# Performance work log

Hardware: AMD Instinct MI355X
Metric: run time of the kernel (lower is better)

Reference implementation:

```python
import jax, jax.numpy as jnp
import numpy as np

C = 256
RED = 8
CR = C // RED  # 32
B, H, W = 4, 64, 64
EPS = 1e-5


def setup_inputs() -> dict:
    key = jax.random.key(0)
    ks = jax.random.split(key, 12)
    s = 0.05
    return {
        "x": jax.random.normal(ks[0], (B, C, H, W), dtype=jnp.float32),
        "Wq": jax.random.normal(ks[1], (CR, C), dtype=jnp.float32) * s,
        "bq": jax.random.normal(ks[2], (CR,), dtype=jnp.float32) * s,
        "Wk": jax.random.normal(ks[3], (CR, C), dtype=jnp.float32) * s,
        "bk": jax.random.normal(ks[4], (CR,), dtype=jnp.float32) * s,
        "Wv": jax.random.normal(ks[5], (C, C), dtype=jnp.float32) * s,
        "bv": jax.random.normal(ks[6], (C,), dtype=jnp.float32) * s,
        "Wo": jax.random.normal(ks[7], (C, C), dtype=jnp.float32) * s,
        "bo": jax.random.normal(ks[8], (C,), dtype=jnp.float32) * s,
        "gamma": jnp.ones((C,), dtype=jnp.float32),
        "beta": jnp.zeros((C,), dtype=jnp.float32),
        "running_mean": jax.random.normal(ks[9], (C,), dtype=jnp.float32) * s,
        "running_var": jax.random.uniform(ks[10], (C,), dtype=jnp.float32, minval=0.5, maxval=1.5),
    }


def reference(x, Wq, bq, Wk, bk, Wv, bv, Wo, bo, gamma, beta, running_mean, running_var):
    b, c, h, w = x.shape
    n = h * w
    scale = c ** (-0.5)  # use_scale=True: in_channels**-0.5
    xf = x.reshape(b, c, n)  # [B, C, N]
    # 1x1 convs == per-pixel channel matmuls
    q = jnp.einsum('oc,bcn->bon', Wq, xf) + bq[None, :, None]   # [B, CR, N]
    k = jnp.einsum('oc,bcn->bon', Wk, xf) + bk[None, :, None]   # [B, CR, N]
    v = jnp.einsum('oc,bcn->bon', Wv, xf) + bv[None, :, None]   # [B, C, N]
    # attention[b, q_pos, k_pos], softmax over key positions (dim=2)
    attn = jnp.einsum('bcq,bck->bqk', q, k) * scale             # [B, N, N]
    attn = jax.nn.softmax(attn, axis=2)
    # out[b, c, q_pos] = sum_k v[b, c, k] * attn[b, q_pos, k]
    out = jnp.einsum('bck,bqk->bcq', v, attn)                   # [B, C, N]
    out = jnp.einsum('oc,bcn->bon', Wo, out) + bo[None, :, None]
    # BatchNorm2d (inference: running stats)
    inv = gamma / jnp.sqrt(running_var + EPS)
    out = out * inv[None, :, None] + (beta - running_mean * inv)[None, :, None]
    out = out.reshape(b, c, h, w)
    return jax.nn.relu(out + x)
```

## Files before the change

### kernel.cpp

```cpp
#include <hip/hip_runtime.h>
#include <hip/hip_bf16.h>

typedef unsigned short u16;
typedef unsigned int u32;

#define B_ 4
#define C_ 256
#define N_ 4096

constexpr float C1 = 0.09016844005556021f;

typedef float f32x16 __attribute__((ext_vector_type(16)));
typedef short bf16x8 __attribute__((ext_vector_type(8)));
typedef u32 u32x4 __attribute__((ext_vector_type(4)));
typedef int i32x2 __attribute__((ext_vector_type(2)));

__device__ __forceinline__ u16 bf16r(float f) {
    union { float f; u32 u; } a; a.f = f;
    u32 u = a.u;
    u += 0x7fffu + ((u >> 16) & 1u);
    return (u16)(u >> 16);
}

__device__ __forceinline__ float bf2f(u16 h) {
    union { u32 u; float f; } a; a.u = ((u32)h) << 16; return a.f;
}

__device__ __forceinline__ u32 pk2(float a, float b) {
    __hip_bfloat162 h = __float22bfloat162_rn(make_float2(a, b));
    union { __hip_bfloat162 h; u32 u; } c; c.h = h;
    return c.u;
}

__device__ __forceinline__ u32 cvtpk(float lo, float hi) {
    u32 r;
    asm("v_cvt_pk_bf16_f32 %0, %1, %2" : "=v"(r) : "v"(lo), "v"(hi));
    return r;
}

__device__ __forceinline__ void swap32(u32 &a, u32 &b) {
#if __has_builtin(__builtin_amdgcn_permlane32_swap)
    i32x2 r = __builtin_amdgcn_permlane32_swap((int)a, (int)b, false, false);
    a = (u32)r.x; b = (u32)r.y;
#else
    u32 as = __shfl_xor(a, 32), bs = __shfl_xor(b, 32);
    int hi = (threadIdx.x & 32) ? 1 : 0;
    u32 na = hi ? bs : a;
    u32 nb = hi ? b : as;
    a = na; b = nb;
#endif
}

__device__ __forceinline__ bf16x8 ld8(const u16* p) {
    return *reinterpret_cast<const bf16x8*>(p);
}

__device__ __forceinline__ void gld_lds16(const u16* g, u16* lbase, int lane) {
#if __has_builtin(__builtin_amdgcn_global_load_lds)
    __builtin_amdgcn_global_load_lds(
        (const __attribute__((address_space(1))) void*)g,
        (__attribute__((address_space(3))) void*)lbase, 16, 0, 0);
#else
    *reinterpret_cast<bf16x8*>(lbase + lane * 8) = ld8(g);
#endif
}

__device__ __forceinline__ int crow(int r, int hi) { return (r & 3) + 8 * (r >> 2) + 4 * hi; }

__global__ __launch_bounds__(256) void prep(
    const float* __restrict__ Wq, const float* __restrict__ Wk,
    const float* __restrict__ Wv, const float* __restrict__ Wo,
    const float* __restrict__ bo, const float* __restrict__ gamma,
    const float* __restrict__ beta, const float* __restrict__ rm, const float* __restrict__ rv,
    u16* __restrict__ wqk, u16* __restrict__ wv_b, u16* __restrict__ wo_b,
    float* __restrict__ scale, float* __restrict__ shift)
{
    int i = blockIdx.x * 256 + threadIdx.x;
    if (i < 16384) {
        float w = (i < 8192) ? Wq[i] * C1 : Wk[i - 8192];
        wqk[i] = bf16r(w);
    } else if (i < 81920) {
        wv_b[i - 16384] = bf16r(Wv[i - 16384]);
    } else if (i < 147456) {
        wo_b[i - 81920] = bf16r(Wo[i - 81920]);
    } else if (i < 147712) {
        int o = i - 147456;
        float inv = gamma[o] * rsqrtf(rv[o] + 1e-5f);
        scale[o] = inv;
        shift[o] = beta[o] + (bo[o] - rm[o]) * inv;
    }
}

__global__ __launch_bounds__(512) void projf(
    const float* __restrict__ x, const u16* __restrict__ wqk, const u16* __restrict__ wv,
    const float* __restrict__ bq, const float* __restrict__ bk, const float* __restrict__ bv,
    u16* __restrict__ qkt, u16* __restrict__ vout)
{
    __shared__ u16 xt[64 * 256];
    int tid = threadIdx.x;
    int lane = tid & 63, wid = tid >> 6;
    int r31 = lane & 31, hi = lane >> 5;
    int b = blockIdx.y, n0 = blockIdx.x * 64;
    const float* xb = x + (size_t)b * C_ * N_ + n0;
#pragma unroll
    for (int i = 0; i < 16; ++i) {
        int c2 = i * 8 + wid;
        int n = lane;
        float a0 = xb[(size_t)(2 * c2) * N_ + n];
        float a1 = xb[(size_t)(2 * c2 + 1) * N_ + n];
        int slot = (c2 >> 2) ^ (n & 31);
        *reinterpret_cast<u32*>(&xt[n * 256 + slot * 8 + (c2 & 3) * 2]) = pk2(a0, a1);
    }
    __syncthreads();
    for (int i = 0; i < 3; ++i) {
        int t = wid + i * 8;
        if (t < 20) {
            bool isqk = (t < 4);
            int nb = isqk ? (t >> 1) * 32 : ((t - 4) & 1) * 32;
            int gb = isqk ? (t & 1) * 32 : ((t - 4) >> 1) * 32;
            const u16* grow = (isqk ? wqk : wv) + (size_t)(gb + r31) * C_ + hi * 8;
            f32x16 acc;
#pragma unroll
            for (int r = 0; r < 16; ++r) acc[r] = 0.f;
#pragma unroll
            for (int ks = 0; ks < 16; ++ks) {
                int slot = (2 * ks + hi) ^ r31;
                bf16x8 lf = ld8(&xt[(nb + r31) * 256 + slot * 8]);
                bf16x8 gf = ld8(grow + ks * 16);
                if (isqk) acc = __builtin_amdgcn_mfma_f32_32x32x16_bf16(lf, gf, acc, 0, 0, 0);
                else      acc = __builtin_amdgcn_mfma_f32_32x32x16_bf16(gf, lf, acc, 0, 0, 0);
            }
            if (isqk) {
                int o = gb + r31;
                float bias = (o < 32) ? bq[o] * C1 : bk[o - 32];
                u16* qrow = qkt + ((size_t)b * N_ + n0 + nb) * 64 + o;
#pragma unroll
                for (int r = 0; r < 16; ++r)
                    qrow[(size_t)crow(r, hi) * 64] = bf16r(acc[r] + bias);
            } else {
                u16* vb = vout + (size_t)b * C_ * N_ + n0 + nb + r31;
#pragma unroll
                for (int r = 0; r < 16; ++r) {
                    int c = gb + crow(r, hi);
                    vb[(size_t)c * N_] = bf16r(acc[r] + bv[c]);
                }
            }
        }
    }
}

__global__ __launch_bounds__(512, 4) void attn(
    const u16* __restrict__ qkt, const u16* __restrict__ v,
    u16* __restrict__ opart, float* __restrict__ lpart, int kts)
{
    __shared__ u16 vt[2][128 * 128];
    __shared__ u16 ktt[2][16 * 128];
    int tid = threadIdx.x;
    int lane = tid & 63, wid = tid >> 6;
    int r31 = lane & 31, hi = lane >> 5;

    int nwg = 32 * 4 * gridDim.z;
    int wgl = blockIdx.x + 32 * (blockIdx.y + 4 * blockIdx.z);
    int cpx = nwg >> 3;
    int swzid = (wgl & 7) * cpx + (wgl >> 3);
    int bx = swzid & 31;
    int by = (swzid >> 5) & 3;
    int bz = swzid >> 7;

    int b = by, zs = bz;
    int q0 = bx * 128 + (wid >> 1) * 32;
    int cb = (wid & 1) * 128;
    const u16* qkb = qkt + (size_t)b * N_ * 64;
    const u16* vbase = v + (size_t)b * C_ * N_;

    int ks_q = tid & 255;
    int ks_row = ks_q >> 4;
    int ks_so = (ks_q & 15) ^ ks_row;
    int ks_k = ks_row * 4 + (ks_so >> 2);
    int ks_d8 = (ks_so & 3) * 8;

    int cpar8 = ((cb + r31) & 1) * 8;
    int vrow0 = (cb + r31) >> 1;
    int vm = vrow0 & 15;
    int kr4 = r31 >> 2;
    int kk3 = (r31 & 3) * 4;

    bf16x8 qf0 = ld8(qkb + (size_t)(q0 + r31) * 64 + hi * 8);
    bf16x8 qf1 = ld8(qkb + (size_t)(q0 + r31) * 64 + 16 + hi * 8);

    f32x16 acc[4];
#pragma unroll
    for (int ct = 0; ct < 4; ++ct)
#pragma unroll
        for (int r = 0; r < 16; ++r) acc[ct][r] = 0.f;

    f32x16 z4;
#pragma unroll
    for (int r = 0; r < 16; ++r) z4[r] = 0.f;

    float l_run = 0.f;
    int ktBeg = zs * kts, ktEnd = (zs + 1) * kts;

    auto stage = [&](int buf, int kt) {
        int k0 = kt * 64;
        if (tid < 256)
            gld_lds16(qkb + (size_t)(k0 + ks_k) * 64 + 32 + ks_d8,
                      &ktt[buf][(size_t)(wid * 64) * 8], lane);
#pragma unroll
        for (int i = 0; i < 4; ++i) {
            int q = i * 512 + tid;
            int row2 = q >> 4;
            int so = (q & 15) ^ (row2 & 15);
            int c = 2 * row2 + (so >> 3);
            int kcol = (so & 7) * 8;
            gld_lds16(vbase + (size_t)c * N_ + k0 + kcol,
                      &vt[buf][(size_t)((i * 512 + wid * 64) * 8)], lane);
        }
    };

    int cur = 0;
    stage(cur, ktBeg);
    __syncthreads();

    for (int kt = ktBeg; kt < ktEnd; ++kt) {
        if (kt + 1 < ktEnd) stage(cur ^ 1, kt + 1);

        float pst = 0.f;
#pragma unroll
        for (int ph = 0; ph < 2; ++ph) {
            int krow = ph * 8 + kr4;
            const u16* kbase = &ktt[cur][krow * 128];
            bf16x8 kf0 = ld8(kbase + (((kk3 + hi) ^ krow) * 8));
            bf16x8 kf1 = ld8(kbase + (((kk3 + 2 + hi) ^ krow) * 8));
            f32x16 s = __builtin_amdgcn_mfma_f32_32x32x16_bf16(kf0, qf0, z4, 0, 0, 0);
            s = __builtin_amdgcn_mfma_f32_32x32x16_bf16(kf1, qf1, s, 0, 0, 0);
            float p[16];
#pragma unroll
            for (int r = 0; r < 16; ++r) { p[r] = __builtin_amdgcn_exp2f(s[r]); pst += p[r]; }
            bf16x8 pf[2];
#pragma unroll
            for (int c16 = 0; c16 < 2; ++c16) {
                u32 w0 = cvtpk(p[8 * c16 + 0], p[8 * c16 + 1]);
                u32 w1 = cvtpk(p[8 * c16 + 2], p[8 * c16 + 3]);
                u32 w2 = cvtpk(p[8 * c16 + 4], p[8 * c16 + 5]);
                u32 w3 = cvtpk(p[8 * c16 + 6], p[8 * c16 + 7]);
                swap32(w0, w2);
                swap32(w1, w3);
                union { bf16x8 f8; u32 u[4]; } fu;
                fu.u[0] = w0; fu.u[1] = w1; fu.u[2] = w2; fu.u[3] = w3;
                pf[c16] = fu.f8;
            }
            int kc0 = ph * 2;
#pragma unroll
            for (int ct = 0; ct < 4; ++ct) {
                const u16* vb2 = &vt[cur][(vrow0 + 16 * ct) * 128];
                bf16x8 vf0 = ld8(vb2 + (((cpar8 + kc0 * 2 + hi) ^ vm) * 8));
                bf16x8 vf1 = ld8(vb2 + (((cpar8 + kc0 * 2 + 2 + hi) ^ vm) * 8));
                acc[ct] = __builtin_amdgcn_mfma_f32_32x32x16_bf16(vf0, pf[0], acc[ct], 0, 0, 0);
                acc[ct] = __builtin_amdgcn_mfma_f32_32x32x16_bf16(vf1, pf[1], acc[ct], 0, 0, 0);
            }
        }
        pst += __shfl_xor(pst, 32);
        l_run += pst;

        __syncthreads();
        cur ^= 1;
    }

    u16* dst = opart + ((size_t)(zs * B_ + b) * N_) * C_;
    if ((wid & 1) == 0 && hi == 0)
        lpart[((size_t)zs * B_ + b) * N_ + q0 + r31] = l_run;
    float (*tls)[32][33] = reinterpret_cast<float (*)[32][33]>(&vt[0][0]);
    int qg = lane >> 4, cd = lane & 15;
#pragma unroll
    for (int ct = 0; ct < 4; ++ct) {
        __syncthreads();
#pragma unroll
        for (int r = 0; r < 16; ++r)
            tls[wid][crow(r, hi)][r31] = acc[ct][r];
        __syncthreads();
#pragma unroll
        for (int it = 0; it < 8; ++it) {
            int qp = it * 4 + qg;
            u32 w = pk2(tls[wid][2 * cd][qp], tls[wid][2 * cd + 1][qp]);
            *reinterpret_cast<u32*>(dst + (size_t)(q0 + qp) * C_ + cb + ct * 32 + 2 * cd) = w;
        }
    }
}

__global__ __launch_bounds__(512) void outprojf(
    const u16* __restrict__ opart, const float* __restrict__ lpart,
    const u16* __restrict__ wo, const float* __restrict__ scl, const float* __restrict__ shf,
    const float* __restrict__ x, float* __restrict__ out, int S)
{
    __shared__ u16 ot[64 * 256];
    __shared__ float linv[64];
    int tid = threadIdx.x;
    int lane = tid & 63, wid = tid >> 6;
    int r31 = lane & 31, hi = lane >> 5;
    int b = blockIdx.y, n0 = blockIdx.x * 64;
    if (tid < 64) {
        float l = 0.f;
        for (int s = 0; s < S; ++s) l += lpart[((size_t)s * B_ + b) * N_ + n0 + tid];
        linv[tid] = 1.f / l;
    }
    __syncthreads();
#pragma unroll
    for (int i = 0; i < 4; ++i) {
        int chunk = i * 512 + tid;
        int n = chunk >> 5, c8 = chunk & 31;
        float a[8];
#pragma unroll
        for (int j = 0; j < 8; ++j) a[j] = 0.f;
        for (int s = 0; s < S; ++s) {
            bf16x8 o = ld8(opart + (((size_t)s * B_ + b) * N_ + n0 + n) * C_ + c8 * 8);
#pragma unroll
            for (int j = 0; j < 8; ++j) a[j] += bf2f((u16)o[j]);
        }
        float li = linv[n];
        u32x4 w;
#pragma unroll
        for (int j = 0; j < 4; ++j) w[j] = pk2(a[2 * j] * li, a[2 * j + 1] * li);
        int sws = c8 ^ (n & 31);
        *reinterpret_cast<u32x4*>(&ot[n * 256 + sws * 8]) = w;
    }
    __syncthreads();
    int obs = wid * 32;
    const u16* arow = wo + (size_t)(obs + r31) * C_ + hi * 8;
    f32x16 acc0, acc1;
#pragma unroll
    for (int r = 0; r < 16; ++r) { acc0[r] = 0.f; acc1[r] = 0.f; }
#pragma unroll
    for (int ks = 0; ks < 16; ++ks) {
        bf16x8 af = ld8(arow + ks * 16);
        int slot = (2 * ks + hi) ^ r31;
        bf16x8 b0 = ld8(&ot[r31 * 256 + slot * 8]);
        bf16x8 b1 = ld8(&ot[(32 + r31) * 256 + slot * 8]);
        acc0 = __builtin_amdgcn_mfma_f32_32x32x16_bf16(af, b0, acc0, 0, 0, 0);
        acc1 = __builtin_amdgcn_mfma_f32_32x32x16_bf16(af, b1, acc1, 0, 0, 0);
    }
    const float* xb = x + (size_t)b * C_ * N_;
    float* op = out + (size_t)b * C_ * N_;
#pragma unroll
    for (int r = 0; r < 16; ++r) {
        int o = obs + crow(r, hi);
        float sc = scl[o], sh = shf[o];
        size_t base = (size_t)o * N_ + n0;
        float v0 = acc0[r] * sc + sh + xb[base + r31];
        op[base + r31] = fmaxf(v0, 0.f);
        float v1 = acc1[r] * sc + sh + xb[base + 32 + r31];
        op[base + 32 + r31] = fmaxf(v1, 0.f);
    }
}

extern "C" void kernel_launch(void* const* d_in, const int* in_sizes, int n_in,
                              void* d_out, int out_size, void* d_ws, size_t ws_size,
                              hipStream_t stream) {
    const float* x     = (const float*)d_in[0];
    const float* Wq    = (const float*)d_in[1];
    const float* bq    = (const float*)d_in[2];
    const float* Wk    = (const float*)d_in[3];
    const float* bk    = (const float*)d_in[4];
    const float* Wv    = (const float*)d_in[5];
    const float* bv    = (const float*)d_in[6];
    const float* Wo    = (const float*)d_in[7];
    const float* bo    = (const float*)d_in[8];
    const float* gamma = (const float*)d_in[9];
    const float* beta  = (const float*)d_in[10];
    const float* rmean = (const float*)d_in[11];
    const float* rvar  = (const float*)d_in[12];
    float* out = (float*)d_out;

    char* ws = (char*)d_ws;
    u16* vbuf = (u16*)(ws);
    u16* qkt  = (u16*)(ws + (size_t)(8u << 20));
    char* wsm = ws + (size_t)(10u << 20);
    u16* wqk  = (u16*)(wsm);
    u16* wv_b = (u16*)(wsm + 32768);
    u16* wo_b = (u16*)(wsm + 32768 + 131072);
    float* scl = (float*)(wsm + 32768 + 262144);
    float* shf = scl + 256;
    float* lpart = (float*)(ws + (size_t)(11u << 20));
    u16* opart = (u16*)(ws + (size_t)(12u << 20));

    size_t need4 = (size_t)(12u << 20) + 4 * (size_t)(8u << 20);
    size_t need2 = (size_t)(12u << 20) + 2 * (size_t)(8u << 20);
    int S = (ws_size >= need4) ? 4 : (ws_size >= need2) ? 2 : 1;

    prep<<<dim3(578), dim3(256), 0, stream>>>(Wq, Wk, Wv, Wo, bo, gamma, beta, rmean, rvar,
                                              wqk, wv_b, wo_b, scl, shf);
    projf<<<dim3(64, 4), dim3(512), 0, stream>>>(x, wqk, wv_b, bq, bk, bv, qkt, vbuf);
    attn<<<dim3(32, 4, S), dim3(512), 0, stream>>>(qkt, vbuf, opart, lpart, 64 / S);
    outprojf<<<dim3(64, 4), dim3(512), 0, stream>>>(opart, lpart, wo_b, scl, shf, x, out, S);
}
```

Measured before the change: 85.69 us.

## Halve projection tiles, add MFMA priority hints, defer row-sum reduction

Projection and output-projection kernels now process 32 pixels per block instead of 64, doubling the grid to 512 blocks so more CUs have work. The attention loop wraps MFMA groups in s_setprio to favour matrix issue across waves, and moves the cross-half row-sum shuffle out of the key loop to run once at the end. The output projection also unrolls the four-split partial sum loads when S is 4. Smaller tiles mean each block reloads the weight rows, so weight traffic per pixel doubles.

```diff
diff --git a/kernel.cpp b/kernel.cpp
--- a/kernel.cpp
+++ b/kernel.cpp
@@ -96,28 +96,28 @@
     const float* __restrict__ bq, const float* __restrict__ bk, const float* __restrict__ bv,
     u16* __restrict__ qkt, u16* __restrict__ vout)
 {
-    __shared__ u16 xt[64 * 256];
+    __shared__ u16 xt[32 * 256];
     int tid = threadIdx.x;
     int lane = tid & 63, wid = tid >> 6;
     int r31 = lane & 31, hi = lane >> 5;
-    int b = blockIdx.y, n0 = blockIdx.x * 64;
+    int b = blockIdx.y, n0 = blockIdx.x * 32;
     const float* xb = x + (size_t)b * C_ * N_ + n0;
 #pragma unroll
-    for (int i = 0; i < 16; ++i) {
-        int c2 = i * 8 + wid;
-        int n = lane;
+    for (int i = 0; i < 8; ++i) {
+        int idx = i * 512 + tid;
+        int n = idx & 31, c2 = idx >> 5;
         float a0 = xb[(size_t)(2 * c2) * N_ + n];
         float a1 = xb[(size_t)(2 * c2 + 1) * N_ + n];
-        int slot = (c2 >> 2) ^ (n & 31);
+        int slot = (c2 >> 2) ^ n;
         *reinterpret_cast<u32*>(&xt[n * 256 + slot * 8 + (c2 & 3) * 2]) = pk2(a0, a1);
     }
     __syncthreads();
-    for (int i = 0; i < 3; ++i) {
+#pragma unroll
+    for (int i = 0; i < 2; ++i) {
         int t = wid + i * 8;
-        if (t < 20) {
-            bool isqk = (t < 4);
-            int nb = isqk ? (t >> 1) * 32 : ((t - 4) & 1) * 32;
-            int gb = isqk ? (t & 1) * 32 : ((t - 4) >> 1) * 32;
+        if (t < 10) {
+            bool isqk = (t < 2);
+            int gb = isqk ? t * 32 : (t - 2) * 32;
             const u16* grow = (isqk ? wqk : wv) + (size_t)(gb + r31) * C_ + hi * 8;
             f32x16 acc;
 #pragma unroll
@@ -125,7 +125,7 @@
 #pragma unroll
             for (int ks = 0; ks < 16; ++ks) {
                 int slot = (2 * ks + hi) ^ r31;
-                bf16x8 lf = ld8(&xt[(nb + r31) * 256 + slot * 8]);
+                bf16x8 lf = ld8(&xt[r31 * 256 + slot * 8]);
                 bf16x8 gf = ld8(grow + ks * 16);
                 if (isqk) acc = __builtin_amdgcn_mfma_f32_32x32x16_bf16(lf, gf, acc, 0, 0, 0);
                 else      acc = __builtin_amdgcn_mfma_f32_32x32x16_bf16(gf, lf, acc, 0, 0, 0);
@@ -133,12 +133,12 @@
             if (isqk) {
                 int o = gb + r31;
                 float bias = (o < 32) ? bq[o] * C1 : bk[o - 32];
-                u16* qrow = qkt + ((size_t)b * N_ + n0 + nb) * 64 + o;
+                u16* qrow = qkt + ((size_t)b * N_ + n0) * 64 + o;
 #pragma unroll
                 for (int r = 0; r < 16; ++r)
                     qrow[(size_t)crow(r, hi) * 64] = bf16r(acc[r] + bias);
             } else {
-                u16* vb = vout + (size_t)b * C_ * N_ + n0 + nb + r31;
+                u16* vb = vout + (size_t)b * C_ * N_ + n0 + r31;
 #pragma unroll
                 for (int r = 0; r < 16; ++r) {
                     int c = gb + crow(r, hi);
@@ -225,18 +225,19 @@
     for (int kt = ktBeg; kt < ktEnd; ++kt) {
         if (kt + 1 < ktEnd) stage(cur ^ 1, kt + 1);
 
-        float pst = 0.f;
 #pragma unroll
         for (int ph = 0; ph < 2; ++ph) {
             int krow = ph * 8 + kr4;
             const u16* kbase = &ktt[cur][krow * 128];
             bf16x8 kf0 = ld8(kbase + (((kk3 + hi) ^ krow) * 8));
             bf16x8 kf1 = ld8(kbase + (((kk3 + 2 + hi) ^ krow) * 8));
+            __builtin_amdgcn_s_setprio(1);
             f32x16 s = __builtin_amdgcn_mfma_f32_32x32x16_bf16(kf0, qf0, z4, 0, 0, 0);
             s = __builtin_amdgcn_mfma_f32_32x32x16_bf16(kf1, qf1, s, 0, 0, 0);
+            __builtin_amdgcn_s_setprio(0);
             float p[16];
 #pragma unroll
-            for (int r = 0; r < 16; ++r) { p[r] = __builtin_amdgcn_exp2f(s[r]); pst += p[r]; }
+            for (int r = 0; r < 16; ++r) { p[r] = __builtin_amdgcn_exp2f(s[r]); l_run += p[r]; }
             bf16x8 pf[2];
 #pragma unroll
             for (int c16 = 0; c16 < 2; ++c16) {
@@ -251,6 +252,7 @@
                 pf[c16] = fu.f8;
             }
             int kc0 = ph * 2;
+            __builtin_amdgcn_s_setprio(1);
 #pragma unroll
             for (int ct = 0; ct < 4; ++ct) {
                 const u16* vb2 = &vt[cur][(vrow0 + 16 * ct) * 128];
@@ -259,13 +261,14 @@
                 acc[ct] = __builtin_amdgcn_mfma_f32_32x32x16_bf16(vf0, pf[0], acc[ct], 0, 0, 0);
                 acc[ct] = __builtin_amdgcn_mfma_f32_32x32x16_bf16(vf1, pf[1], acc[ct], 0, 0, 0);
             }
+            __builtin_amdgcn_s_setprio(0);
         }
-        pst += __shfl_xor(pst, 32);
-        l_run += pst;
 
         __syncthreads();
         cur ^= 1;
     }
+
+    l_run += __shfl_xor(l_run, 32);
 
     u16* dst = opart + ((size_t)(zs * B_ + b) * N_) * C_;
     if ((wid & 1) == 0 && hi == 0)
@@ -293,51 +296,61 @@
     const u16* __restrict__ wo, const float* __restrict__ scl, const float* __restrict__ shf,
     const float* __restrict__ x, float* __restrict__ out, int S)
 {
-    __shared__ u16 ot[64 * 256];
-    __shared__ float linv[64];
+    __shared__ u16 ot[32 * 256];
+    __shared__ float linv[32];
     int tid = threadIdx.x;
     int lane = tid & 63, wid = tid >> 6;
     int r31 = lane & 31, hi = lane >> 5;
-    int b = blockIdx.y, n0 = blockIdx.x * 64;
-    if (tid < 64) {
+    int b = blockIdx.y, n0 = blockIdx.x * 32;
+    if (tid < 32) {
         float l = 0.f;
         for (int s = 0; s < S; ++s) l += lpart[((size_t)s * B_ + b) * N_ + n0 + tid];
         linv[tid] = 1.f / l;
     }
     __syncthreads();
-#pragma unroll
-    for (int i = 0; i < 4; ++i) {
+    const size_t sstr = (size_t)B_ * N_ * C_;
+#pragma unroll
+    for (int i = 0; i < 2; ++i) {
         int chunk = i * 512 + tid;
         int n = chunk >> 5, c8 = chunk & 31;
+        const u16* base = opart + ((size_t)b * N_ + n0 + n) * C_ + c8 * 8;
         float a[8];
-#pragma unroll
-        for (int j = 0; j < 8; ++j) a[j] = 0.f;
-        for (int s = 0; s < S; ++s) {
-            bf16x8 o = ld8(opart + (((size_t)s * B_ + b) * N_ + n0 + n) * C_ + c8 * 8);
-#pragma unroll
-            for (int j = 0; j < 8; ++j) a[j] += bf2f((u16)o[j]);
+        if (S == 4) {
+            bf16x8 o0 = ld8(base);
+            bf16x8 o1 = ld8(base + sstr);
+            bf16x8 o2 = ld8(base + 2 * sstr);
+            bf16x8 o3 = ld8(base + 3 * sstr);
+#pragma unroll
+            for (int j = 0; j < 8; ++j)
+                a[j] = (bf2f((u16)o0[j]) + bf2f((u16)o1[j])) + (bf2f((u16)o2[j]) + bf2f((u16)o3[j]));
+        } else {
+#pragma unroll
+            for (int j = 0; j < 8; ++j) a[j] = 0.f;
+            for (int s = 0; s < S; ++s) {
+                bf16x8 o = ld8(base + s * sstr);
+#pragma unroll
+                for (int j = 0; j < 8; ++j) a[j] += bf2f((u16)o[j]);
+            }
         }
         float li = linv[n];
         u32x4 w;
 #pragma unroll
         for (int j = 0; j < 4; ++j) w[j] = pk2(a[2 * j] * li, a[2 * j + 1] * li);
-        int sws = c8 ^ (n & 31);
+        int sws = c8 ^ n;
         *reinterpret_cast<u32x4*>(&ot[n * 256 + sws * 8]) = w;
     }
     __syncthreads();
     int obs = wid * 32;
     const u16* arow = wo + (size_t)(obs + r31) * C_ + hi * 8;
-    f32x16 acc0, acc1;
-#pragma unroll
-    for (int r = 0; r < 16; ++r) { acc0[r] = 0.f; acc1[r] = 0.f; }
+    f32x16 acc;
+#pragma unroll
+    for (int r = 0; r < 16; ++r) acc[r] = 0.f;
 #pragma unroll
     for (int ks = 0; ks < 16; ++ks) {
         bf16x8 af = ld8(arow + ks * 16);
         int slot = (2 * ks + hi) ^ r31;
-        bf16x8 b0 = ld8(&ot[r31 * 256 + slot * 8]);
-        bf16x8 b1 = ld8(&ot[(32 + r31) * 256 + slot * 8]);
-        acc0 = __builtin_amdgcn_mfma_f32_32x32x16_bf16(af, b0, acc0, 0, 0, 0);
-        acc1 = __builtin_amdgcn_mfma_f32_32x32x16_bf16(af, b1, acc1, 0, 0, 0);
+        bf16x8 bf = ld8(&ot[r31 * 256 + slot * 8]);
+        acc = __builtin_amdgcn_mfma_f32_32x32x16_bf16(af, bf, acc, 0, 0, 0);
     }
     const float* xb = x + (size_t)b * C_ * N_;
     float* op = out + (size_t)b * C_ * N_;
@@ -346,10 +359,8 @@
         int o = obs + crow(r, hi);
         float sc = scl[o], sh = shf[o];
         size_t base = (size_t)o * N_ + n0;
-        float v0 = acc0[r] * sc + sh + xb[base + r31];
+        float v0 = acc[r] * sc + sh + xb[base + r31];
         op[base + r31] = fmaxf(v0, 0.f);
-        float v1 = acc1[r] * sc + sh + xb[base + 32 + r31];
-        op[base + 32 + r31] = fmaxf(v1, 0.f);
     }
 }
 
@@ -389,7 +400,7 @@
 
     prep<<<dim3(578), dim3(256), 0, stream>>>(Wq, Wk, Wv, Wo, bo, gamma, beta, rmean, rvar,
                                               wqk, wv_b, wo_b, scl, shf);
-    projf<<<dim3(64, 4), dim3(512), 0, stream>>>(x, wqk, wv_b, bq, bk, bv, qkt, vbuf);
+    projf<<<dim3(128, 4), dim3(512), 0, stream>>>(x, wqk, wv_b, bq, bk, bv, qkt, vbuf);
     attn<<<dim3(32, 4, S), dim3(512), 0, stream>>>(qkt, vbuf, opart, lpart, 64 / S);
-    outprojf<<<dim3(64, 4), dim3(512), 0, stream>>>(opart, lpart, wo_b, scl, shf, x, out, S);
-}
+    outprojf<<<dim3(128, 4), dim3(512), 0, stream>>>(opart, lpart, wo_b, scl, shf, x, out, S);
+}
```

Result: no change. 86.64 us (+1.1%).
